# Kernel optimization log

Hardware: AMD Instinct MI355X
Metric: run time of the kernel (lower is better)

The kernel has to match this reference:

```python
import jax, jax.numpy as jnp
import numpy as np

BATCH = 1024
INPUT_DIM = 4096
HV_DIM = 8192          # == 2**NUM_QUBITS, so encode_classical fully overwrites the state
NUM_QUBITS = 13
QUANTUM_DEPTH = 3


def setup_inputs() -> dict:
    key = jax.random.key(0)
    k1, k2, k3 = jax.random.split(key, 3)
    x = jax.random.normal(k1, (BATCH, INPUT_DIM), dtype=jnp.float32)
    # torch nn.Linear weight layout: [out_features, in_features]
    W = jax.random.normal(k2, (HV_DIM, INPUT_DIM), dtype=jnp.float32)
    quantum_params = jax.random.normal(k3, (QUANTUM_DEPTH, NUM_QUBITS), dtype=jnp.float32)
    return {"x": x, "W": W, "quantum_params": quantum_params}


def reference(x, W, quantum_params):
    # projection: classical_hv = x @ W^T  -> [B, HV_DIM]
    classical = x @ W.T
    # encode_classical: normalize, cast to complex, renormalize (second norm is 1;
    # kept for fidelity with the original code path)
    amps = (classical / jnp.linalg.norm(classical, axis=-1, keepdims=True)).astype(jnp.complex64)
    amps = amps / jnp.linalg.norm(amps, axis=-1, keepdims=True)

    # sequential gate sequence: for depth in range(D): for qubit in range(Q):
    #   amps = amps*cos(a/2) + roll(amps, 1)*sin(a/2)*1j
    # each step uses the updated amplitudes -> lax.scan over the flattened angles
    angles = quantum_params.reshape(-1)  # [D*Q], depth-major matching the loop order

    def step(a, angle):
        c = jnp.cos(angle * 0.5)
        s = jnp.sin(angle * 0.5)
        return a * c + jnp.roll(a, 1, axis=-1) * (s * 1j), None

    amps, _ = jax.lax.scan(step, amps, angles)
    return amps  # [B, 2**NUM_QUBITS] complex64 quantum amplitudes
```

## Files before the change

kernel.cpp:

```cpp
#include <hip/hip_runtime.h>
#include <hip/hip_fp16.h>
#include <math.h>

typedef _Float16 half8 __attribute__((ext_vector_type(8)));
typedef __fp16 fp16x2 __attribute__((ext_vector_type(2)));
typedef float f32x4 __attribute__((ext_vector_type(4)));

#define BATCH 1024
#define IN_DIM 4096
#define HV 8192
#define NTAP 40

#define BM 128
#define BN 128
#define BK 32
#define BKP 36

#define GLD16(g, l) __builtin_amdgcn_global_load_lds(                          \
    (const __attribute__((address_space(1))) void*)(g),                        \
    (__attribute__((address_space(3))) void*)(l), 16, 0, 0)

static __device__ __forceinline__ half8 pk8(f32x4 a, f32x4 b) {
    union { fp16x2 p[4]; half8 h; } u;
    u.p[0] = __builtin_amdgcn_cvt_pkrtz(a.x, a.y);
    u.p[1] = __builtin_amdgcn_cvt_pkrtz(a.z, a.w);
    u.p[2] = __builtin_amdgcn_cvt_pkrtz(b.x, b.y);
    u.p[3] = __builtin_amdgcn_cvt_pkrtz(b.z, b.w);
    return u.h;
}

typedef _Float16 half4v __attribute__((ext_vector_type(4)));
__global__ __launch_bounds__(256) void cvt_f32_f16(const float4* __restrict__ src,
                                                   half4v* __restrict__ dst, int n4) {
    int i = blockIdx.x * 256 + threadIdx.x;
    if (i < n4) {
        float4 v = src[i];
        half4v h;
        h.x = (_Float16)v.x; h.y = (_Float16)v.y;
        h.z = (_Float16)v.z; h.w = (_Float16)v.w;
        dst[i] = h;
    }
}

__global__ __launch_bounds__(64) void compute_taps(const float* __restrict__ qp,
                                                   float* __restrict__ taps) {
    const int lane = threadIdx.x;
    float qv = (lane < 39) ? qp[lane] : 0.f;
    float pr = (lane == 0) ? 1.f : 0.f;
    float pim = 0.f;
    for (int t = 0; t < 39; t++) {
        float a = __shfl(qv, t, 64) * 0.5f;
        float c = cosf(a), s = sinf(a);
        float ur = __shfl_up(pr, 1, 64);
        float ui = __shfl_up(pim, 1, 64);
        if (lane == 0) { ur = 0.f; ui = 0.f; }
        float nr = c * pr - s * ui;
        float ni = c * pim + s * ur;
        pr = nr; pim = ni;
    }
    if (lane < NTAP) taps[lane] = pr;
}

__global__ __launch_bounds__(512, 4) void gemm_f16(
        const _Float16* __restrict__ A,
        const _Float16* __restrict__ B,
        float* __restrict__ out,
        long out_n) {
    __shared__ __align__(16) _Float16 lgA[BM * BK];
    __shared__ __align__(16) _Float16 lgB[BN * BK];

    const int tid  = threadIdx.x;
    const int lane = tid & 63;
    const int wave = tid >> 6;
    const int wm = wave & 1;
    const int wn = wave >> 1;
    const int q = lane >> 4, r = lane & 15;
    const int bm = blockIdx.y * BM;
    const int bn = blockIdx.x * BN;

    const int srow  = tid >> 2;
    const int sslot = (tid & 3) ^ ((srow >> 1) & 3);
    const _Float16* gA = A + (size_t)(bm + srow) * IN_DIM + sslot * 8;
    const _Float16* gB = B + (size_t)(bn + srow) * IN_DIM + sslot * 8;
    _Float16* lA = &lgA[(wave * 16) * BK];
    _Float16* lB = &lgB[(wave * 16) * BK];

    f32x4 acc[4][2] = {};

    for (int k0 = 0; k0 < IN_DIM; k0 += BK) {
        GLD16(gA + k0, lA);
        GLD16(gB + k0, lB);
        __syncthreads();

        half8 af[4], bf[2];
        #pragma unroll
        for (int i = 0; i < 4; i++) {
            const int R = wm * 64 + i * 16 + r;
            af[i] = *(const half8*)&lgA[R * BK + ((q ^ ((R >> 1) & 3)) * 8)];
        }
        #pragma unroll
        for (int j = 0; j < 2; j++) {
            const int R = wn * 32 + j * 16 + r;
            bf[j] = *(const half8*)&lgB[R * BK + ((q ^ ((R >> 1) & 3)) * 8)];
        }

        #pragma unroll
        for (int i = 0; i < 4; i++)
            #pragma unroll
            for (int j = 0; j < 2; j++)
                acc[i][j] = __builtin_amdgcn_mfma_f32_16x16x32_f16(af[i], bf[j], acc[i][j], 0, 0, 0);
        __syncthreads();
    }

    #pragma unroll
    for (int i = 0; i < 4; i++) {
        const int row = bm + wm * 64 + i * 16 + q * 4;
        #pragma unroll
        for (int j = 0; j < 2; j++) {
            const int col = bn + wn * 32 + j * 16 + r;
            #pragma unroll
            for (int reg = 0; reg < 4; reg++) {
                long idx = (long)(row + reg) * HV + col;
                if (idx < out_n) out[idx] = acc[i][j][reg];
            }
        }
    }
}

__global__ __launch_bounds__(256) void gemm_f32in(
        const float* __restrict__ A, const float* __restrict__ B,
        float* __restrict__ out, long out_n) {
    __shared__ __align__(16) float lgA[BM * BKP];
    __shared__ __align__(16) float lgB[BN * BKP];

    const int tid  = threadIdx.x;
    const int lane = tid & 63;
    const int wave = tid >> 6;
    const int wm = wave & 1, wn = wave >> 1;
    const int q = lane >> 4, r = lane & 15;
    const int bm = blockIdx.y * BM;
    const int bn = blockIdx.x * BN;

    const int rg = lane >> 3;
    const int cg = (lane & 7) * 4;
    const float* gA = A + (size_t)(bm + wave * 32 + rg) * IN_DIM + cg;
    const float* gB = B + (size_t)(bn + wave * 32 + rg) * IN_DIM + cg;
    float* lA = &lgA[(wave * 32 + rg) * BKP + cg];
    float* lB = &lgB[(wave * 32 + rg) * BKP + cg];

    f32x4 acc[4][4] = {};

    for (int k0 = 0; k0 < IN_DIM; k0 += BK) {
        float4 va[4], vb[4];
        #pragma unroll
        for (int i = 0; i < 4; i++) {
            va[i] = *(const float4*)(gA + k0 + (size_t)(8 * i) * IN_DIM);
            vb[i] = *(const float4*)(gB + k0 + (size_t)(8 * i) * IN_DIM);
        }
        __syncthreads();
        #pragma unroll
        for (int i = 0; i < 4; i++) {
            *(float4*)(lA + 8 * i * BKP) = va[i];
            *(float4*)(lB + 8 * i * BKP) = vb[i];
        }
        __syncthreads();

        half8 af[4], bf[4];
        #pragma unroll
        for (int i = 0; i < 4; i++) {
            const float* p = &lgA[(wm * 64 + i * 16 + r) * BKP + q * 8];
            af[i] = pk8(*(const f32x4*)p, *(const f32x4*)(p + 4));
        }
        #pragma unroll
        for (int j = 0; j < 4; j++) {
            const float* p = &lgB[(wn * 64 + j * 16 + r) * BKP + q * 8];
            bf[j] = pk8(*(const f32x4*)p, *(const f32x4*)(p + 4));
        }

        #pragma unroll
        for (int i = 0; i < 4; i++)
            #pragma unroll
            for (int j = 0; j < 4; j++)
                acc[i][j] = __builtin_amdgcn_mfma_f32_16x16x32_f16(af[i], bf[j], acc[i][j], 0, 0, 0);
    }

    #pragma unroll
    for (int i = 0; i < 4; i++) {
        const int row = bm + wm * 64 + i * 16 + q * 4;
        #pragma unroll
        for (int j = 0; j < 4; j++) {
            const int col = bn + wn * 64 + j * 16 + r;
            #pragma unroll
            for (int reg = 0; reg < 4; reg++) {
                long idx = (long)(row + reg) * HV + col;
                if (idx < out_n) out[idx] = acc[i][j][reg];
            }
        }
    }
}

__global__ __launch_bounds__(256) void norm_conv(float* __restrict__ out,
                                                 const float* __restrict__ qp,
                                                 const float* __restrict__ taps,
                                                 long out_n) {
    __shared__ __align__(16) float ldsv[HV + 48];
    __shared__ float scr[NTAP];
    __shared__ float red[4];

    const int b = blockIdx.x;
    if ((long)(b + 1) * HV > out_n) return;

    const int tid = threadIdx.x;
    const int lane = tid & 63;
    const int wave = tid >> 6;
    float* rowp = out + (size_t)b * HV;
    const float4* row4 = (const float4*)rowp;
    float4* l4 = (float4*)ldsv;

    float ss = 0.f;
    #pragma unroll
    for (int it = 0; it < 8; it++) {
        int j = it * 256 + tid;
        float4 v = row4[j];
        ss += v.x * v.x + v.y * v.y + v.z * v.z + v.w * v.w;
        l4[10 + j] = v;
    }
    if (tid < NTAP) ldsv[tid] = rowp[HV - NTAP + tid];

    #pragma unroll
    for (int off = 32; off > 0; off >>= 1) ss += __shfl_down(ss, off, 64);
    if (lane == 0) red[wave] = ss;

    if (taps) {
        if (tid < NTAP) scr[tid] = taps[tid];
    } else if (wave == 0) {
        float qv = (lane < 39) ? qp[lane] : 0.f;
        float pr = (lane == 0) ? 1.f : 0.f;
        float pim = 0.f;
        for (int t = 0; t < 39; t++) {
            float a = __shfl(qv, t, 64) * 0.5f;
            float c = cosf(a), s = sinf(a);
            float ur = __shfl_up(pr, 1, 64);
            float ui = __shfl_up(pim, 1, 64);
            if (lane == 0) { ur = 0.f; ui = 0.f; }
            float nr = c * pr - s * ui;
            float ni = c * pim + s * ur;
            pr = nr; pim = ni;
        }
        if (lane < NTAP) scr[lane] = pr;
    }
    __syncthreads();

    const float inv = 1.0f / sqrtf(red[0] + red[1] + red[2] + red[3]);
    float rc[NTAP];
    #pragma unroll
    for (int k = 0; k < NTAP; k++) rc[k] = scr[k] * inv;

    float4* out4 = (float4*)rowp;
    #pragma unroll
    for (int it = 0; it < 8; it++) {
        const int i0 = (it * 256 + tid) * 4;
        float w[48];
        #pragma unroll
        for (int t = 0; t < 12; t++) ((float4*)w)[t] = l4[(i0 >> 2) + t];

        float ar[4] = {0.f, 0.f, 0.f, 0.f};
        #pragma unroll
        for (int k = 0; k < NTAP; k++) {
            const float c0 = rc[k];
            #pragma unroll
            for (int o = 0; o < 4; o++)
                ar[o] += c0 * w[o + NTAP - k];
        }
        out4[i0 >> 2] = make_float4(ar[0], ar[1], ar[2], ar[3]);
    }
}

extern "C" void kernel_launch(void* const* d_in, const int* in_sizes, int n_in,
                              void* d_out, int out_size, void* d_ws, size_t ws_size,
                              hipStream_t stream) {
    const float* x  = (const float*)d_in[0];
    const float* W  = (const float*)d_in[1];
    const float* qp = (const float*)d_in[2];
    float* out = (float*)d_out;
    long out_n = (long)out_size;

    const size_t need = (size_t)BATCH * IN_DIM * 2 + (size_t)HV * IN_DIM * 2;
    dim3 grid(HV / BN, BATCH / BM);

    if (ws_size >= need) {
        _Float16* xh = (_Float16*)d_ws;
        _Float16* wh = xh + (size_t)BATCH * IN_DIM;
        float* taps = nullptr;
        if (ws_size >= need + 256) {
            taps = (float*)((char*)d_ws + need);
            compute_taps<<<1, 64, 0, stream>>>(qp, taps);
        }
        int n4x = BATCH * IN_DIM / 4;
        int n4w = HV * IN_DIM / 4;
        cvt_f32_f16<<<n4x / 256, 256, 0, stream>>>((const float4*)x, (half4v*)xh, n4x);
        cvt_f32_f16<<<n4w / 256, 256, 0, stream>>>((const float4*)W, (half4v*)wh, n4w);
        gemm_f16<<<grid, 512, 0, stream>>>(xh, wh, out, out_n);
        norm_conv<<<BATCH, 256, 0, stream>>>(out, qp, taps, out_n);
    } else {
        float* taps = nullptr;
        if (ws_size >= 256) {
            taps = (float*)d_ws;
            compute_taps<<<1, 64, 0, stream>>>(qp, taps);
        }
        gemm_f32in<<<grid, 256, 0, stream>>>(x, W, out, out_n);
        norm_conv<<<BATCH, 256, 0, stream>>>(out, qp, taps, out_n);
    }
}
```

Baseline: 330.3 us.

## Double-buffer fp16 GEMM with larger per-wave tiles and restructure norm_conv reuse

The fp16 GEMM drops from 512 to 256 threads per block, gives each wave a 64x64 output tile instead of 64x32, and double-buffers LDS so the async global-to-LDS load of the next K slice overlaps the MFMAs on the current one. The aim is to hide global load latency and raise MFMA work per LDS read, at the cost of more accumulator registers and lower occupancy. norm_conv now computes 32 contiguous outputs per thread from one 72-element window held in registers, and swizzles the LDS row buffer to avoid bank conflicts. This cuts redundant LDS window loads, and the normalisation is folded into the final store.

```diff
diff --git a/kernel.cpp b/kernel.cpp
--- a/kernel.cpp
+++ b/kernel.cpp
@@ -61,13 +61,13 @@
     if (lane < NTAP) taps[lane] = pr;
 }
 
-__global__ __launch_bounds__(512, 4) void gemm_f16(
+__global__ __launch_bounds__(256, 2) void gemm_f16(
         const _Float16* __restrict__ A,
         const _Float16* __restrict__ B,
         float* __restrict__ out,
         long out_n) {
-    __shared__ __align__(16) _Float16 lgA[BM * BK];
-    __shared__ __align__(16) _Float16 lgB[BN * BK];
+    __shared__ __align__(16) _Float16 lgA[2][BM * BK];
+    __shared__ __align__(16) _Float16 lgB[2][BN * BK];
 
     const int tid  = threadIdx.x;
     const int lane = tid & 63;
@@ -80,44 +80,60 @@
 
     const int srow  = tid >> 2;
     const int sslot = (tid & 3) ^ ((srow >> 1) & 3);
-    const _Float16* gA = A + (size_t)(bm + srow) * IN_DIM + sslot * 8;
-    const _Float16* gB = B + (size_t)(bn + srow) * IN_DIM + sslot * 8;
-    _Float16* lA = &lgA[(wave * 16) * BK];
-    _Float16* lB = &lgB[(wave * 16) * BK];
-
-    f32x4 acc[4][2] = {};
-
-    for (int k0 = 0; k0 < IN_DIM; k0 += BK) {
-        GLD16(gA + k0, lA);
-        GLD16(gB + k0, lB);
+    const _Float16* gA0 = A + (size_t)(bm + srow) * IN_DIM + sslot * 8;
+    const _Float16* gA1 = gA0 + (size_t)64 * IN_DIM;
+    const _Float16* gB0 = B + (size_t)(bn + srow) * IN_DIM + sslot * 8;
+    const _Float16* gB1 = gB0 + (size_t)64 * IN_DIM;
+    const int d0 = (wave * 16) * BK;
+    const int d1 = (64 + wave * 16) * BK;
+
+    f32x4 acc[4][4] = {};
+
+#define STAGE(buf, k0)  do {                         \
+        GLD16(gA0 + (k0), &lgA[buf][d0]);            \
+        GLD16(gA1 + (k0), &lgA[buf][d1]);            \
+        GLD16(gB0 + (k0), &lgB[buf][d0]);            \
+        GLD16(gB1 + (k0), &lgB[buf][d1]);            \
+    } while (0)
+
+#define COMPUTE(buf)  do {                                                         \
+        half8 af[4], bf[4];                                                        \
+        _Pragma("unroll")                                                          \
+        for (int i = 0; i < 4; i++) {                                              \
+            const int R = wm * 64 + i * 16 + r;                                    \
+            af[i] = *(const half8*)&lgA[buf][R * BK + ((q ^ ((R >> 1) & 3)) * 8)]; \
+        }                                                                          \
+        _Pragma("unroll")                                                          \
+        for (int j = 0; j < 4; j++) {                                              \
+            const int R = wn * 64 + j * 16 + r;                                    \
+            bf[j] = *(const half8*)&lgB[buf][R * BK + ((q ^ ((R >> 1) & 3)) * 8)]; \
+        }                                                                          \
+        _Pragma("unroll")                                                          \
+        for (int i = 0; i < 4; i++)                                                \
+            _Pragma("unroll")                                                      \
+            for (int j = 0; j < 4; j++)                                            \
+                acc[i][j] = __builtin_amdgcn_mfma_f32_16x16x32_f16(af[i], bf[j], acc[i][j], 0, 0, 0); \
+    } while (0)
+
+    STAGE(0, 0);
+    __syncthreads();
+    for (int k0 = 0; k0 < IN_DIM; k0 += 2 * BK) {
+        STAGE(1, k0 + BK);
+        COMPUTE(0);
         __syncthreads();
-
-        half8 af[4], bf[2];
-        #pragma unroll
-        for (int i = 0; i < 4; i++) {
-            const int R = wm * 64 + i * 16 + r;
-            af[i] = *(const half8*)&lgA[R * BK + ((q ^ ((R >> 1) & 3)) * 8)];
-        }
-        #pragma unroll
-        for (int j = 0; j < 2; j++) {
-            const int R = wn * 32 + j * 16 + r;
-            bf[j] = *(const half8*)&lgB[R * BK + ((q ^ ((R >> 1) & 3)) * 8)];
-        }
-
-        #pragma unroll
-        for (int i = 0; i < 4; i++)
-            #pragma unroll
-            for (int j = 0; j < 2; j++)
-                acc[i][j] = __builtin_amdgcn_mfma_f32_16x16x32_f16(af[i], bf[j], acc[i][j], 0, 0, 0);
+        if (k0 + 2 * BK < IN_DIM) STAGE(0, k0 + 2 * BK);
+        COMPUTE(1);
         __syncthreads();
     }
+#undef STAGE
+#undef COMPUTE
 
     #pragma unroll
     for (int i = 0; i < 4; i++) {
         const int row = bm + wm * 64 + i * 16 + q * 4;
         #pragma unroll
-        for (int j = 0; j < 2; j++) {
-            const int col = bn + wn * 32 + j * 16 + r;
+        for (int j = 0; j < 4; j++) {
+            const int col = bn + wn * 64 + j * 16 + r;
             #pragma unroll
             for (int reg = 0; reg < 4; reg++) {
                 long idx = (long)(row + reg) * HV + col;
@@ -199,11 +215,12 @@
     }
 }
 
+#define SW4(p4) ((p4) ^ (((p4) >> 3) & 7))
 __global__ __launch_bounds__(256) void norm_conv(float* __restrict__ out,
                                                  const float* __restrict__ qp,
                                                  const float* __restrict__ taps,
                                                  long out_n) {
-    __shared__ __align__(16) float ldsv[HV + 48];
+    __shared__ __align__(16) float ldsv[40 + HV + 24];
     __shared__ float scr[NTAP];
     __shared__ float red[4];
 
@@ -223,9 +240,11 @@
         int j = it * 256 + tid;
         float4 v = row4[j];
         ss += v.x * v.x + v.y * v.y + v.z * v.z + v.w * v.w;
-        l4[10 + j] = v;
-    }
-    if (tid < NTAP) ldsv[tid] = rowp[HV - NTAP + tid];
+        l4[SW4(10 + j)] = v;
+    }
+    if (tid < NTAP) {
+        ldsv[(SW4(tid >> 2) << 2) | (tid & 3)] = rowp[HV - NTAP + tid];
+    }
 
     #pragma unroll
     for (int off = 32; off > 0; off >>= 1) ss += __shfl_down(ss, off, 64);
@@ -252,27 +271,26 @@
     __syncthreads();
 
     const float inv = 1.0f / sqrtf(red[0] + red[1] + red[2] + red[3]);
-    float rc[NTAP];
-    #pragma unroll
-    for (int k = 0; k < NTAP; k++) rc[k] = scr[k] * inv;
+
+    float w[72];
+    #pragma unroll
+    for (int t = 0; t < 18; t++) ((float4*)w)[t] = l4[SW4(8 * tid + t)];
 
     float4* out4 = (float4*)rowp;
     #pragma unroll
-    for (int it = 0; it < 8; it++) {
-        const int i0 = (it * 256 + tid) * 4;
-        float w[48];
-        #pragma unroll
-        for (int t = 0; t < 12; t++) ((float4*)w)[t] = l4[(i0 >> 2) + t];
-
-        float ar[4] = {0.f, 0.f, 0.f, 0.f};
+    for (int h = 0; h < 2; h++) {
+        float av[16] = {};
         #pragma unroll
         for (int k = 0; k < NTAP; k++) {
-            const float c0 = rc[k];
+            const float c = scr[k];
             #pragma unroll
-            for (int o = 0; o < 4; o++)
-                ar[o] += c0 * w[o + NTAP - k];
-        }
-        out4[i0 >> 2] = make_float4(ar[0], ar[1], ar[2], ar[3]);
+            for (int o = 0; o < 16; o++) av[o] += c * w[40 + h * 16 + o - k];
+        }
+        #pragma unroll
+        for (int t = 0; t < 4; t++) {
+            out4[8 * tid + 4 * h + t] = make_float4(inv * av[4 * t], inv * av[4 * t + 1],
+                                                    inv * av[4 * t + 2], inv * av[4 * t + 3]);
+        }
     }
 }
 
@@ -300,7 +318,7 @@
         int n4w = HV * IN_DIM / 4;
         cvt_f32_f16<<<n4x / 256, 256, 0, stream>>>((const float4*)x, (half4v*)xh, n4x);
         cvt_f32_f16<<<n4w / 256, 256, 0, stream>>>((const float4*)W, (half4v*)wh, n4w);
-        gemm_f16<<<grid, 512, 0, stream>>>(xh, wh, out, out_n);
+        gemm_f16<<<grid, 256, 0, stream>>>(xh, wh, out, out_n);
         norm_conv<<<BATCH, 256, 0, stream>>>(out, qp, taps, out_n);
     } else {
         float* taps = nullptr;
```

New measurement: 321.2 us. -2.8%, faster.
